# Optimization experiments

Measured on AMD Instinct MI355X. Metric: run time of the kernel, lower is better.

Reference implementation:

```python
import jax, jax.numpy as jnp
import numpy as np

EPS = 1e-5

def _fm(x):
    # feature_map: exact (erf) GELU + 1, matching torch F.gelu default
    return jax.nn.gelu(x, approximate=False) + 1.0

def _gds(q, k):
    # global_dot_score: reduce over seq dim, broadcast back over seq
    e = (q * k).sum(axis=1)            # [B, D]
    return e[:, None, :] * q           # [B, S, D]

def _attn(q, k, v, scale):
    qf = _fm(q)
    kf = _fm(k)
    e = _gds(qf, kf) / scale           # [B, S, D]
    return jax.nn.softmax(e, axis=1) * v

def _ln(x, g, b):
    mu = x.mean(axis=-1, keepdims=True)
    var = ((x - mu) ** 2).mean(axis=-1, keepdims=True)
    return (x - mu) / jnp.sqrt(var + EPS) * g + b

def setup_inputs() -> dict:
    B, S, D, V, L, O = 8, 2048, 1024, 32000, 2, 2
    key = jax.random.key(0)
    ks = jax.random.split(key, 4)
    src = jax.random.randint(ks[0], (B, S), 0, V, dtype=jnp.int64 if jax.config.jax_enable_x64 else jnp.int32)
    trg = jax.random.randint(ks[1], (B, S), 0, V, dtype=src.dtype)
    emb = jax.random.normal(ks[2], (V, D), dtype=jnp.float32) * 0.02
    Wc = jax.random.normal(ks[3], (D, O), dtype=jnp.float32) * 0.02
    return {
        'src': src, 'trg': trg, 'emb': emb,
        'enc_g': jnp.ones((L, D), jnp.float32), 'enc_b': jnp.zeros((L, D), jnp.float32),
        'dec_ng': jnp.ones((L, D), jnp.float32), 'dec_nb': jnp.zeros((L, D), jnp.float32),
        'dec_tg': jnp.ones((L, D), jnp.float32), 'dec_tb': jnp.zeros((L, D), jnp.float32),
        'Wc': Wc, 'bc': jnp.zeros((O,), jnp.float32),
    }

def reference(src, trg, emb, enc_g, enc_b, dec_ng, dec_nb, dec_tg, dec_tb, Wc, bc):
    D = emb.shape[1]
    L = enc_g.shape[0]
    scale = jnp.sqrt(jnp.asarray(D, emb.dtype))

    # ---------- Encoder ----------
    x = emb[src]                          # [B, S, D]
    ctx = jnp.cumsum(x, axis=1)
    out = _gds(x, ctx)                    # encoder: out becomes rep
    rep = out
    for i in range(L):
        a = _attn(out, ctx, rep, scale)
        out = _ln(a + out, enc_g[i], enc_b[i])
        if i < L - 1:
            ctx = jnp.cumsum(out, axis=1)
            rep = _gds(out, ctx)
    enc_out = out
    enc_ctx = ctx[:, -1:, :]              # [B, 1, D]

    # ---------- Decoder ----------
    xe = emb[trg]
    ctx = jnp.cumsum(xe, axis=1)
    x = _gds(xe, ctx)                     # decoder: x becomes rep
    rep = x
    k2 = enc_ctx                          # [B, 1, D]
    v2 = enc_out.sum(axis=1, keepdims=True)  # [B, 1, D]
    for i in range(L):
        a1 = _attn(x, ctx, rep, scale)
        q = _ln(a1 + x, dec_ng[i], dec_nb[i])
        a2 = _attn(q, k2, v2, scale)      # cross attention (broadcast over seq)
        x = _ln(a2 + q, dec_tg[i], dec_tb[i])
        if i < L - 1:
            ctx = jnp.cumsum(x, axis=1)
            rep = _gds(x, ctx)

    # ---------- Predictor (use='seq', pool='mean') ----------
    pooled = x.mean(axis=1)               # [B, D]
    return pooled @ Wc + bc               # [B, out]
```

## Files before the change

kernel.cpp:

```cpp
#include <hip/hip_runtime.h>
#include <math.h>

namespace {

constexpr int Bb = 8;
constexpr int Ss = 2048;
constexpr int Dd = 1024;
constexpr int D4 = Dd / 4;
constexpr int NC = 128;
constexpr int Sc2 = Ss / NC;
constexpr int Tb = 256;
constexpr int SEG = 8;
constexpr int CPS = NC / SEG;
constexpr float INV_SCALE = 0.03125f;
constexpr float BIG = 3.0e38f;

__device__ __forceinline__ float fast_erf(float z) {
  float az = fabsf(z);
  float t = __builtin_amdgcn_rcpf(fmaf(0.3275911f, az, 1.0f));
  float p = fmaf(1.061405429f, t, -1.453152027f);
  p = fmaf(p, t, 1.421413741f);
  p = fmaf(p, t, -0.284496736f);
  p = fmaf(p, t, 0.254829592f);
  p *= t;
  float e = __expf(-az * az);
  float r = fmaf(-p, e, 1.0f);
  return copysignf(r, z);
}
__device__ __forceinline__ float fm_act(float x) {
  return fmaf(0.5f * x, 1.0f + fast_erf(x * 0.70710678118654752f), 1.0f);
}

__device__ __forceinline__ float4 f4(float v) { return make_float4(v, v, v, v); }
__device__ __forceinline__ float4 add4(float4 a, float4 b) {
  return make_float4(a.x + b.x, a.y + b.y, a.z + b.z, a.w + b.w);
}
__device__ __forceinline__ float4 mul4(float4 a, float4 b) {
  return make_float4(a.x * b.x, a.y * b.y, a.z * b.z, a.w * b.w);
}
__device__ __forceinline__ float4 fma4(float4 a, float4 b, float4 c) {
  return make_float4(fmaf(a.x, b.x, c.x), fmaf(a.y, b.y, c.y), fmaf(a.z, b.z, c.z), fmaf(a.w, b.w, c.w));
}
__device__ __forceinline__ float4 min4(float4 a, float4 b) {
  return make_float4(fminf(a.x, b.x), fminf(a.y, b.y), fminf(a.z, b.z), fminf(a.w, b.w));
}
__device__ __forceinline__ float4 max4(float4 a, float4 b) {
  return make_float4(fmaxf(a.x, b.x), fmaxf(a.y, b.y), fmaxf(a.z, b.z), fmaxf(a.w, b.w));
}
__device__ __forceinline__ float4 fm4(float4 x) {
  return make_float4(fm_act(x.x), fm_act(x.y), fm_act(x.z), fm_act(x.w));
}
__device__ __forceinline__ float4 ld4(const float* p, size_t j4) {
  return reinterpret_cast<const float4*>(p)[j4];
}
__device__ __forceinline__ void st4(float* p, size_t j4, float4 v) {
  reinterpret_cast<float4*>(p)[j4] = v;
}
__device__ __forceinline__ float4 pexp4(float4 ei, float4 qf, float4 M) {
  return make_float4(__expf(fmaf(ei.x, qf.x, -M.x)), __expf(fmaf(ei.y, qf.y, -M.y)),
                     __expf(fmaf(ei.z, qf.z, -M.z)), __expf(fmaf(ei.w, qf.w, -M.w)));
}

__device__ __forceinline__ float blockSum(float v) {
  __shared__ float wsm[Tb / 64];
  for (int off = 32; off > 0; off >>= 1) v += __shfl_down(v, off, 64);
  const int lane = threadIdx.x & 63;
  const int w = threadIdx.x >> 6;
  __syncthreads();
  if (lane == 0) wsm[w] = v;
  __syncthreads();
  return wsm[0] + wsm[1] + wsm[2] + wsm[3];
}

struct GA { const int* tok; float* X; float* cs; float* el; };
struct SA { const float* cs; const float* el; float* off; float* e; float* last; };
struct PA { const float* X; const float* qs; const float* off; float* pe; float* pmn; float* pmx; };
struct MA { const float* pe; const float* pmn; const float* pmx; const float* k2; float* ei; float* Mv; };
struct QA { const float* X; const float* qs; const float* ei; const float* Mv; float* ps; };
struct RA { const float* pp; float* outv; int recip; };
struct LA { float* X; const float* qs; const float* vs; const float* rs; const float* ml;
            const float* ei; const float* Mv; const float* rdv; const float* g; const float* bt;
            float* cs; float* el; float* xe; float* xn; float* xx; int wout; };


__global__ __launch_bounds__(Tb) void k_gather(GA a0, GA a1, const float* __restrict__ emb) {
  const GA a = (blockIdx.z == 0) ? a0 : a1;
  const int t = threadIdx.x, c = blockIdx.x, b = blockIdx.y;
  const int* tp = a.tok + b * Ss + c * Sc2;
  float4* xp = reinterpret_cast<float4*>(a.X) + ((size_t)(b * Ss + c * Sc2)) * D4 + t;
  const float4* ep = reinterpret_cast<const float4*>(emb);
  float4 run = f4(0.f), e = f4(0.f);
#pragma unroll
  for (int i = 0; i < Sc2; ++i) {
    float4 v = ep[(size_t)tp[i] * D4 + t];
    xp[(size_t)i * D4] = v;
    run = add4(run, v);
    e = fma4(v, run, e);
  }
  const size_t idx = ((size_t)b * NC + c) * D4 + t;
  st4(a.cs, idx, run);
  st4(a.el, idx, e);
}

__global__ __launch_bounds__(Tb) void k_p1(PA a0, PA a1) {
  const PA a = (blockIdx.z == 0) ? a0 : a1;
  const int t = threadIdx.x, c = blockIdx.x, b = blockIdx.y;
  const size_t idx = ((size_t)b * NC + c) * D4 + t;
  float4 run = ld4(a.off, idx);
  const float4 q4 = a.qs ? ld4(a.qs, (size_t)b * D4 + t) : f4(1.f);
  const float4* xp = reinterpret_cast<const float4*>(a.X) + ((size_t)(b * Ss + c * Sc2)) * D4 + t;
  float4 e = f4(0.f), mn = f4(BIG), mx = f4(0.f);
#pragma unroll
  for (int i = 0; i < Sc2; ++i) {
    float4 x = xp[(size_t)i * D4];
    run = add4(run, x);
    float4 qf = fm4(mul4(q4, x));
    float4 kf = fm4(run);
    e = fma4(qf, kf, e);
    mn = min4(mn, qf);
    mx = max4(mx, qf);
  }
  st4(a.pe, idx, e);
  st4(a.pmn, idx, mn);
  st4(a.pmx, idx, mx);
}

__global__ __launch_bounds__(Tb) void k_p2(QA a0, QA a1) {
  const QA a = (blockIdx.z == 0) ? a0 : a1;
  const int t = threadIdx.x, c = blockIdx.x, b = blockIdx.y;
  const size_t j4 = (size_t)b * D4 + t;
  const float4 q4 = a.qs ? ld4(a.qs, j4) : f4(1.f);
  const float4 e4 = ld4(a.ei, j4);
  const float4 M4 = ld4(a.Mv, j4);
  const float4* xp = reinterpret_cast<const float4*>(a.X) + ((size_t)(b * Ss + c * Sc2)) * D4 + t;
  float4 s = f4(0.f);
#pragma unroll
  for (int i = 0; i < Sc2; ++i) {
    float4 x = xp[(size_t)i * D4];
    float4 qf = fm4(mul4(q4, x));
    s = add4(s, pexp4(e4, qf, M4));
  }
  st4(a.ps, ((size_t)b * NC + c) * D4 + t, s);
}

__global__ __launch_bounds__(Tb) void k_ln(LA a0, LA a1) {
  const LA a = (blockIdx.z == 0) ? a0 : a1;
  __shared__ float red[Sc2][Tb];
  __shared__ float mu_s[Sc2], inv_s[Sc2];
  const int t = threadIdx.x, c = blockIdx.x, b = blockIdx.y;
  float4* xp = reinterpret_cast<float4*>(a.X) + ((size_t)(b * Ss + c * Sc2)) * D4 + t;
  const size_t j4 = (size_t)b * D4 + t;
  const float4 e4 = ld4(a.ei, j4), M4 = ld4(a.Mv, j4), rv4 = ld4(a.rdv, j4);
  const float4 q4 = a.qs ? ld4(a.qs, j4) : f4(1.f);
  const float4 vs4 = a.vs ? ld4(a.vs, j4) : f4(1.f);
  const float4 ml4 = a.ml ? ld4(a.ml, j4) : f4(1.f);
  const float4 rs4 = a.rs ? ld4(a.rs, j4) : f4(1.f);
  float4 vals[Sc2];
#pragma unroll
  for (int i = 0; i < Sc2; ++i) {
    float4 x = xp[(size_t)i * D4];
    float4 qf = fm4(mul4(q4, x));
    float4 p = mul4(pexp4(e4, qf, M4), rv4);
    float4 v = a.ml ? mul4(p, ml4) : mul4(p, mul4(vs4, x));
    float4 val = add4(v, mul4(rs4, x));
    vals[i] = val;
    red[i][t] = val.x + val.y + val.z + val.w;
  }
  __syncthreads();
  const int lane = t & 63, w = t >> 6;
#pragma unroll
  for (int rr = 0; rr < Sc2 / 4; ++rr) {
    const int row = w * (Sc2 / 4) + rr;
    float s = red[row][lane] + red[row][lane + 64] + red[row][lane + 128] + red[row][lane + 192];
    for (int off = 32; off > 0; off >>= 1) s += __shfl_down(s, off, 64);
    if (lane == 0) mu_s[row] = s * (1.0f / Dd);
  }
  __syncthreads();
#pragma unroll
  for (int i = 0; i < Sc2; ++i) {
    const float m = mu_s[i];
    float4 vv = vals[i];
    float aa = vv.x - m, b2 = vv.y - m, c2 = vv.z - m, d2 = vv.w - m;
    red[i][t] = aa * aa + b2 * b2 + c2 * c2 + d2 * d2;
  }
  __syncthreads();
#pragma unroll
  for (int rr = 0; rr < Sc2 / 4; ++rr) {
    const int row = w * (Sc2 / 4) + rr;
    float s = red[row][lane] + red[row][lane + 64] + red[row][lane + 128] + red[row][lane + 192];
    for (int off = 32; off > 0; off >>= 1) s += __shfl_down(s, off, 64);
    if (lane == 0) inv_s[row] = rsqrtf(s * (1.0f / Dd) + 1e-5f);
  }
  __syncthreads();
  const float4 g4 = ld4(a.g, t), b4 = ld4(a.bt, t);
  float4 run = f4(0.f), e = f4(0.f);
  float4 xs = f4(0.f), xmn = f4(BIG), xmx = f4(0.f);
#pragma unroll
  for (int i = 0; i < Sc2; ++i) {
    const float m = mu_s[i], inv = inv_s[i];
    float4 vv = vals[i];
    float4 y;
    y.x = fmaf((vv.x - m) * inv, g4.x, b4.x);
    y.y = fmaf((vv.y - m) * inv, g4.y, b4.y);
    y.z = fmaf((vv.z - m) * inv, g4.z, b4.z);
    y.w = fmaf((vv.w - m) * inv, g4.w, b4.w);
    if (a.wout) xp[(size_t)i * D4] = y;
    if (a.cs) {
      run = add4(run, y);
      if (a.el) e = fma4(y, run, e);
    }
    if (a.xe) {
      float4 qfy = fm4(y);
      xs = add4(xs, qfy);
      xmn = min4(xmn, qfy);
      xmx = max4(xmx, qfy);
    }
  }
  const size_t idx = ((size_t)b * NC + c) * D4 + t;
  if (a.cs) st4(a.cs, idx, run);
  if (a.el) st4(a.el, idx, e);
  if (a.xe) {
    st4(a.xe, idx, xs);
    st4(a.xn, idx, xmn);
    st4(a.xx, idx, xmx);
  }
}


__global__ __launch_bounds__(Tb) void t_scan8(SA a0, SA a1) {
  const SA a = (blockIdx.z == 0) ? a0 : a1;
  __shared__ float lds[SEG][32];
  const int tid = threadIdx.x;
  const int jl = tid & 31, seg = tid >> 5;
  const int j = blockIdx.x * 32 + jl;
  const int b = j >> 10, d = j & 1023;
  const size_t base = (size_t)b * NC * Dd + d;
  float s = 0.f;
#pragma unroll 8
  for (int i = 0; i < CPS; ++i) s += a.cs[base + (size_t)(seg * CPS + i) * Dd];
  lds[seg][jl] = s;
  __syncthreads();
  float o = 0.f;
#pragma unroll
  for (int g2 = 0; g2 < SEG; ++g2) { float v = lds[g2][jl]; o += (g2 < seg) ? v : 0.f; }
  __syncthreads();
  float run = o, e = 0.f;
#pragma unroll 8
  for (int i = 0; i < CPS; ++i) {
    const size_t k = base + (size_t)(seg * CPS + i) * Dd;
    float cv = a.cs[k];
    a.off[k] = run;
    e += a.el[k] + run * cv;
    run += cv;
  }
  lds[seg][jl] = e;
  __syncthreads();
  if (seg == 0) {
    float et = 0.f;
#pragma unroll
    for (int g2 = 0; g2 < SEG; ++g2) et += lds[g2][jl];
    a.e[j] = et;
  }
  if (a.last && seg == SEG - 1) a.last[j] = run;
}

__global__ __launch_bounds__(Tb) void t_m8(MA a0, MA a1) {
  const MA a = (blockIdx.z == 0) ? a0 : a1;
  __shared__ float le[SEG][32], lmn[SEG][32], lmx[SEG][32];
  const int tid = threadIdx.x;
  const int jl = tid & 31, seg = tid >> 5;
  const int j = blockIdx.x * 32 + jl;
  const int b = j >> 10, d = j & 1023;
  const size_t base = (size_t)b * NC * Dd + d;
  float ec = 0.f, mn = BIG, mx = 0.f;
#pragma unroll 8
  for (int i = 0; i < CPS; ++i) {
    const size_t k = base + (size_t)(seg * CPS + i) * Dd;
    ec += a.pe[k];
    mn = fminf(mn, a.pmn[k]);
    mx = fmaxf(mx, a.pmx[k]);
  }
  le[seg][jl] = ec; lmn[seg][jl] = mn; lmx[seg][jl] = mx;
  __syncthreads();
  if (seg == 0) {
#pragma unroll
    for (int g2 = 1; g2 < SEG; ++g2) {
      ec += le[g2][jl];
      mn = fminf(mn, lmn[g2][jl]);
      mx = fmaxf(mx, lmx[g2][jl]);
    }
    if (a.k2) ec *= fm_act(a.k2[j]);
    const float e2 = ec * INV_SCALE;
    a.ei[j] = e2;
    a.Mv[j] = (ec >= 0.f) ? e2 * mx : e2 * mn;
  }
}

__global__ __launch_bounds__(Tb) void t_red8(RA a0, RA a1) {
  const RA a = (blockIdx.z == 0) ? a0 : a1;
  __shared__ float lds[SEG][32];
  const int tid = threadIdx.x;
  const int jl = tid & 31, seg = tid >> 5;
  const int j = blockIdx.x * 32 + jl;
  const int b = j >> 10, d = j & 1023;
  const size_t base = (size_t)b * NC * Dd + d;
  float s = 0.f;
#pragma unroll 8
  for (int i = 0; i < CPS; ++i) s += a.pp[base + (size_t)(seg * CPS + i) * Dd];
  lds[seg][jl] = s;
  __syncthreads();
  if (seg == 0) {
#pragma unroll
    for (int g2 = 1; g2 < SEG; ++g2) s += lds[g2][jl];
    a.outv[j] = a.recip ? 1.0f / s : s;
  }
}

__global__ __launch_bounds__(Tb) void k_final(const float* __restrict__ pooled, const float* __restrict__ Wc,
    const float* __restrict__ bc, float* __restrict__ out) {
  const int b = blockIdx.x, t = threadIdx.x;
  float4 acc = ld4(pooled, (size_t)b * D4 + t);
  float4 w0 = ld4(Wc, 2 * t), w1 = ld4(Wc, 2 * t + 1);
  float s0 = acc.x * w0.x + acc.y * w0.z + acc.z * w1.x + acc.w * w1.z;
  float s1 = acc.x * w0.y + acc.y * w0.w + acc.z * w1.y + acc.w * w1.w;
  s0 = blockSum(s0);
  s1 = blockSum(s1);
  if (t == 0) {
    out[b * 2 + 0] = s0 * (1.0f / Ss) + bc[0];
    out[b * 2 + 1] = s1 * (1.0f / Ss) + bc[1];
  }
}

}

extern "C" void kernel_launch(void* const* d_in, const int* in_sizes, int n_in,
                              void* d_out, int out_size, void* d_ws, size_t ws_size,
                              hipStream_t stream) {
  (void)in_sizes; (void)n_in; (void)out_size; (void)ws_size;
  const int* src = (const int*)d_in[0];
  const int* trg = (const int*)d_in[1];
  const float* emb = (const float*)d_in[2];
  const float* enc_g = (const float*)d_in[3];
  const float* enc_b = (const float*)d_in[4];
  const float* dec_ng = (const float*)d_in[5];
  const float* dec_nb = (const float*)d_in[6];
  const float* dec_tg = (const float*)d_in[7];
  const float* dec_tb = (const float*)d_in[8];
  const float* Wc = (const float*)d_in[9];
  const float* bc = (const float*)d_in[10];
  float* out = (float*)d_out;

  float* ws = (float*)d_ws;
  const size_t TEN = (size_t)Bb * Ss * Dd;
  const size_t MM = (size_t)Bb * NC * Dd;
  float* A0 = ws;
  float* A1 = A0 + TEN;
  float* p = A1 + TEN;
  float* csE = p; p += MM;  float* elE = p; p += MM;  float* offE = p; p += MM;
  float* peE = p; p += MM;  float* pmnE = p; p += MM; float* pmxE = p; p += MM;
  float* psE = p; p += MM;
  float* csD = p; p += MM;  float* elD = p; p += MM;  float* offD = p; p += MM;
  float* peD = p; p += MM;  float* pmnD = p; p += MM; float* pmxD = p; p += MM;
  float* psD = p; p += MM;
  const int BD = Bb * Dd;
  float* e0E = p; p += BD;  float* e1E = p; p += BD;
  float* e0D = p; p += BD;  float* e1D = p; p += BD;
  float* eiE = p; p += BD;  float* MvE = p; p += BD;  float* rdvE = p; p += BD;
  float* eiD = p; p += BD;  float* MvD = p; p += BD;  float* rdvD = p; p += BD;
  float* ectx = p; p += BD; float* v2 = p; p += BD;   float* pooled = p; p += BD;

  const dim3 g2(NC, Bb, 2), g1(NC, Bb, 1);
  const dim3 t2(BD / 32, 1, 2), t1(BD / 32, 1, 1);

  k_gather<<<g2, Tb, 0, stream>>>(GA{src, A0, csE, elE}, GA{trg, A1, csD, elD}, emb);
  t_scan8<<<t2, Tb, 0, stream>>>(SA{csE, elE, offE, e0E, nullptr}, SA{csD, elD, offD, e0D, nullptr});
  k_p1<<<g2, Tb, 0, stream>>>(PA{A0, e0E, offE, peE, pmnE, pmxE}, PA{A1, e0D, offD, peD, pmnD, pmxD});
  t_m8<<<t2, Tb, 0, stream>>>(MA{peE, pmnE, pmxE, nullptr, eiE, MvE}, MA{peD, pmnD, pmxD, nullptr, eiD, MvD});
  k_p2<<<g2, Tb, 0, stream>>>(QA{A0, e0E, eiE, MvE, psE}, QA{A1, e0D, eiD, MvD, psD});
  t_red8<<<t2, Tb, 0, stream>>>(RA{psE, rdvE, 1}, RA{psD, rdvD, 1});
  k_ln<<<g2, Tb, 0, stream>>>(
      LA{A0, e0E, e0E, e0E, nullptr, eiE, MvE, rdvE, enc_g, enc_b, csE, elE, nullptr, nullptr, nullptr, 1},
      LA{A1, e0D, e0D, e0D, nullptr, eiD, MvD, rdvD, dec_ng, dec_nb, nullptr, nullptr, peD, pmnD, pmxD, 1});

  t_scan8<<<t1, Tb, 0, stream>>>(SA{csE, elE, offE, e1E, ectx}, SA{csE, elE, offE, e1E, ectx});
  k_p1<<<g1, Tb, 0, stream>>>(PA{A0, nullptr, offE, peE, pmnE, pmxE}, PA{A0, nullptr, offE, peE, pmnE, pmxE});

  t_m8<<<t2, Tb, 0, stream>>>(MA{peE, pmnE, pmxE, nullptr, eiE, MvE}, MA{peD, pmnD, pmxD, ectx, eiD, MvD});
  k_p2<<<g2, Tb, 0, stream>>>(QA{A0, nullptr, eiE, MvE, psE}, QA{A1, nullptr, eiD, MvD, psD});
  t_red8<<<t2, Tb, 0, stream>>>(RA{psE, rdvE, 1}, RA{psD, rdvD, 1});
  k_ln<<<g1, Tb, 0, stream>>>(
      LA{A0, nullptr, e1E, nullptr, nullptr, eiE, MvE, rdvE, enc_g + Dd, enc_b + Dd, csE, nullptr, nullptr, nullptr, nullptr, 0},
      LA{A0, nullptr, e1E, nullptr, nullptr, eiE, MvE, rdvE, enc_g + Dd, enc_b + Dd, csE, nullptr, nullptr, nullptr, nullptr, 0});
  t_red8<<<t1, Tb, 0, stream>>>(RA{csE, v2, 0}, RA{csE, v2, 0});

  k_ln<<<g1, Tb, 0, stream>>>(
      LA{A1, nullptr, nullptr, nullptr, v2, eiD, MvD, rdvD, dec_tg, dec_tb, csD, elD, nullptr, nullptr, nullptr, 1},
      LA{A1, nullptr, nullptr, nullptr, v2, eiD, MvD, rdvD, dec_tg, dec_tb, csD, elD, nullptr, nullptr, nullptr, 1});

  t_scan8<<<t1, Tb, 0, stream>>>(SA{csD, elD, offD, e1D, nullptr}, SA{csD, elD, offD, e1D, nullptr});
  k_p1<<<g1, Tb, 0, stream>>>(PA{A1, nullptr, offD, peD, pmnD, pmxD}, PA{A1, nullptr, offD, peD, pmnD, pmxD});
  t_m8<<<t1, Tb, 0, stream>>>(MA{peD, pmnD, pmxD, nullptr, eiD, MvD}, MA{peD, pmnD, pmxD, nullptr, eiD, MvD});
  k_p2<<<g1, Tb, 0, stream>>>(QA{A1, nullptr, eiD, MvD, psD}, QA{A1, nullptr, eiD, MvD, psD});
  t_red8<<<t1, Tb, 0, stream>>>(RA{psD, rdvD, 1}, RA{psD, rdvD, 1});
  k_ln<<<g1, Tb, 0, stream>>>(
      LA{A1, nullptr, e1D, nullptr, nullptr, eiD, MvD, rdvD, dec_ng + Dd, dec_nb + Dd, nullptr, nullptr, peD, pmnD, pmxD, 1},
      LA{A1, nullptr, e1D, nullptr, nullptr, eiD, MvD, rdvD, dec_ng + Dd, dec_nb + Dd, nullptr, nullptr, peD, pmnD, pmxD, 1});

  t_m8<<<t1, Tb, 0, stream>>>(MA{peD, pmnD, pmxD, ectx, eiD, MvD}, MA{peD, pmnD, pmxD, ectx, eiD, MvD});
  k_p2<<<g1, Tb, 0, stream>>>(QA{A1, nullptr, eiD, MvD, psD}, QA{A1, nullptr, eiD, MvD, psD});
  t_red8<<<t1, Tb, 0, stream>>>(RA{psD, rdvD, 1}, RA{psD, rdvD, 1});
  k_ln<<<g1, Tb, 0, stream>>>(
      LA{A1, nullptr, nullptr, nullptr, v2, eiD, MvD, rdvD, dec_tg + Dd, dec_tb + Dd, csD, nullptr, nullptr, nullptr, nullptr, 0},
      LA{A1, nullptr, nullptr, nullptr, v2, eiD, MvD, rdvD, dec_tg + Dd, dec_tb + Dd, csD, nullptr, nullptr, nullptr, nullptr, 0});

  t_red8<<<t1, Tb, 0, stream>>>(RA{csD, pooled, 0}, RA{csD, pooled, 0});
  k_final<<<Bb, Tb, 0, stream>>>(pooled, Wc, bc, out);
}
```

Baseline: 421.6 us.

## Fuse chunk-offset scan into p1 pass and vectorize token loads in gather

```diff
diff --git a/kernel.cpp b/kernel.cpp
--- a/kernel.cpp
+++ b/kernel.cpp
@@ -86,13 +86,19 @@
 __global__ __launch_bounds__(Tb) void k_gather(GA a0, GA a1, const float* __restrict__ emb) {
   const GA a = (blockIdx.z == 0) ? a0 : a1;
   const int t = threadIdx.x, c = blockIdx.x, b = blockIdx.y;
-  const int* tp = a.tok + b * Ss + c * Sc2;
+  const int4* tp4 = reinterpret_cast<const int4*>(a.tok + b * Ss + c * Sc2);
+  int toks[Sc2];
+#pragma unroll
+  for (int k = 0; k < Sc2 / 4; ++k) {
+    int4 v = tp4[k];
+    toks[4 * k] = v.x; toks[4 * k + 1] = v.y; toks[4 * k + 2] = v.z; toks[4 * k + 3] = v.w;
+  }
   float4* xp = reinterpret_cast<float4*>(a.X) + ((size_t)(b * Ss + c * Sc2)) * D4 + t;
   const float4* ep = reinterpret_cast<const float4*>(emb);
   float4 run = f4(0.f), e = f4(0.f);
 #pragma unroll
   for (int i = 0; i < Sc2; ++i) {
-    float4 v = ep[(size_t)tp[i] * D4 + t];
+    float4 v = ep[(size_t)toks[i] * D4 + t];
     xp[(size_t)i * D4] = v;
     run = add4(run, v);
     e = fma4(v, run, e);
@@ -123,6 +129,45 @@
   st4(a.pe, idx, e);
   st4(a.pmn, idx, mn);
   st4(a.pmx, idx, mx);
+}
+
+__global__ __launch_bounds__(Tb) void k_p1scan(const float* __restrict__ X, const float* __restrict__ cs,
+    const float* __restrict__ el, float* __restrict__ pe, float* __restrict__ pmn, float* __restrict__ pmx,
+    float* __restrict__ eout, float* __restrict__ ectx) {
+  const int t = threadIdx.x, c = blockIdx.x, b = blockIdx.y;
+  const size_t cbase = (size_t)b * NC * D4 + t;
+  float4 run = f4(0.f);
+  if (c == NC - 1) {
+    float4 e = f4(0.f), myoff = f4(0.f);
+    for (int cc = 0; cc < NC; ++cc) {
+      float4 v = ld4(cs, cbase + (size_t)cc * D4);
+      if (cc == NC - 1) myoff = run;
+      e = add4(e, fma4(run, v, ld4(el, cbase + (size_t)cc * D4)));
+      run = add4(run, v);
+    }
+    const size_t j4 = (size_t)b * D4 + t;
+    st4(eout, j4, e);
+    if (ectx) st4(ectx, j4, run);
+    run = myoff;
+  } else {
+    for (int cc = 0; cc < c; ++cc) run = add4(run, ld4(cs, cbase + (size_t)cc * D4));
+  }
+  const size_t idx = ((size_t)b * NC + c) * D4 + t;
+  const float4* xp = reinterpret_cast<const float4*>(X) + ((size_t)(b * Ss + c * Sc2)) * D4 + t;
+  float4 e = f4(0.f), mn = f4(BIG), mx = f4(0.f);
+#pragma unroll
+  for (int i = 0; i < Sc2; ++i) {
+    float4 x = xp[(size_t)i * D4];
+    run = add4(run, x);
+    float4 qf = fm4(x);
+    float4 kf = fm4(run);
+    e = fma4(qf, kf, e);
+    mn = min4(mn, qf);
+    mx = max4(mx, qf);
+  }
+  st4(pe, idx, e);
+  st4(pmn, idx, mn);
+  st4(pmx, idx, mx);
 }
 
 __global__ __launch_bounds__(Tb) void k_p2(QA a0, QA a1) {
@@ -382,8 +427,7 @@
       LA{A0, e0E, e0E, e0E, nullptr, eiE, MvE, rdvE, enc_g, enc_b, csE, elE, nullptr, nullptr, nullptr, 1},
       LA{A1, e0D, e0D, e0D, nullptr, eiD, MvD, rdvD, dec_ng, dec_nb, nullptr, nullptr, peD, pmnD, pmxD, 1});
 
-  t_scan8<<<t1, Tb, 0, stream>>>(SA{csE, elE, offE, e1E, ectx}, SA{csE, elE, offE, e1E, ectx});
-  k_p1<<<g1, Tb, 0, stream>>>(PA{A0, nullptr, offE, peE, pmnE, pmxE}, PA{A0, nullptr, offE, peE, pmnE, pmxE});
+  k_p1scan<<<g1, Tb, 0, stream>>>(A0, csE, elE, peE, pmnE, pmxE, e1E, ectx);
 
   t_m8<<<t2, Tb, 0, stream>>>(MA{peE, pmnE, pmxE, nullptr, eiE, MvE}, MA{peD, pmnD, pmxD, ectx, eiD, MvD});
   k_p2<<<g2, Tb, 0, stream>>>(QA{A0, nullptr, eiE, MvE, psE}, QA{A1, nullptr, eiD, MvD, psD});
@@ -397,8 +441,7 @@
       LA{A1, nullptr, nullptr, nullptr, v2, eiD, MvD, rdvD, dec_tg, dec_tb, csD, elD, nullptr, nullptr, nullptr, 1},
       LA{A1, nullptr, nullptr, nullptr, v2, eiD, MvD, rdvD, dec_tg, dec_tb, csD, elD, nullptr, nullptr, nullptr, 1});
 
-  t_scan8<<<t1, Tb, 0, stream>>>(SA{csD, elD, offD, e1D, nullptr}, SA{csD, elD, offD, e1D, nullptr});
-  k_p1<<<g1, Tb, 0, stream>>>(PA{A1, nullptr, offD, peD, pmnD, pmxD}, PA{A1, nullptr, offD, peD, pmnD, pmxD});
+  k_p1scan<<<g1, Tb, 0, stream>>>(A1, csD, elD, peD, pmnD, pmxD, e1D, nullptr);
   t_m8<<<t1, Tb, 0, stream>>>(MA{peD, pmnD, pmxD, nullptr, eiD, MvD}, MA{peD, pmnD, pmxD, nullptr, eiD, MvD});
   k_p2<<<g1, Tb, 0, stream>>>(QA{A1, nullptr, eiD, MvD, psD}, QA{A1, nullptr, eiD, MvD, psD});
   t_red8<<<t1, Tb, 0, stream>>>(RA{psD, rdvD, 1}, RA{psD, rdvD, 1});
```

New measurement: 476.4 us. 13.0% more time.
